# Optimization experiments

Measured on AMD Instinct MI355X. Metric: run time of the kernel, lower is better.

Reference implementation:

```python
import jax, jax.numpy as jnp
import numpy as np

N_NODES = 100000
N_EDGES = 1200000
L = 4  # message-passing layers
SLOPE = 0.01  # nn.LeakyReLU default negative slope


def leaky(v):
    return jnp.where(v >= 0, v, SLOPE * v)


def layer_norm(h, g, b, eps=1e-5):
    mu = jnp.mean(h, axis=-1, keepdims=True)
    var = jnp.var(h, axis=-1, keepdims=True)
    return (h - mu) * jax.lax.rsqrt(var + eps) * g + b


def setup_inputs() -> dict:
    key = jax.random.key(0)
    ks = jax.random.split(key, 20)
    s = 0.05
    return {
        "x": jax.random.normal(ks[0], (N_NODES, 16), jnp.float32),
        "pos": jax.random.uniform(ks[1], (N_NODES, 3), jnp.float32),
        "edge_src": jax.random.randint(ks[2], (N_EDGES,), 0, N_NODES),
        "edge_dst": jax.random.randint(ks[3], (N_EDGES,), 0, N_NODES),
        "edge_w": jax.random.uniform(ks[4], (N_EDGES,), jnp.float32),
        "enc_W1": jax.random.normal(ks[5], (16, 128), jnp.float32) * s,
        "enc_b1": jax.random.normal(ks[6], (128,), jnp.float32) * s,
        "enc_W2": jax.random.normal(ks[7], (128, 64), jnp.float32) * s,
        "enc_b2": jax.random.normal(ks[8], (64,), jnp.float32) * s,
        "dec_W1": jax.random.normal(ks[9], (64, 24), jnp.float32) * s,
        "dec_b1": jax.random.normal(ks[10], (24,), jnp.float32) * s,
        "dec_W2": jax.random.normal(ks[11], (24, 3), jnp.float32) * s,
        "dec_b2": jax.random.normal(ks[12], (3,), jnp.float32) * s,
        "ln_g": jnp.ones((L, 64), jnp.float32),
        "ln_b": jnp.zeros((L, 64), jnp.float32),
        "node_W": jax.random.normal(ks[13], (L, 64, 32), jnp.float32) * s,
        "node_b": jax.random.normal(ks[14], (L, 32), jnp.float32) * s,
        "edge_W": jax.random.normal(ks[15], (L, 64, 32), jnp.float32) * s,
        "edge_b": jax.random.normal(ks[16], (L, 32), jnp.float32) * s,
        "mlp_W": jax.random.normal(ks[17], (L, 32, 64), jnp.float32) * s,
        "mlp_b": jax.random.normal(ks[18], (L, 64), jnp.float32) * s,
    }


def reference(x, pos, edge_src, edge_dst, edge_w,
              enc_W1, enc_b1, enc_W2, enc_b2,
              dec_W1, dec_b1, dec_W2, dec_b2,
              ln_g, ln_b, node_W, node_b, edge_W, edge_b, mlp_W, mlp_b):
    n = x.shape[0]
    # node_encoder: Linear -> LeakyReLU -> Linear
    h = leaky(x @ enc_W1 + enc_b1) @ enc_W2 + enc_b2  # [N, 64]
    for l in range(L):
        hn = layer_norm(h, ln_g[l], ln_b[l])  # [N, 64]
        # edge-weighted scatter-sum: m_e = w_e * h_src, aggregate into dst
        msg = jax.ops.segment_sum(edge_w[:, None] * hn[edge_src], edge_dst,
                                  num_segments=n)  # [N, 64]
        y = (hn @ node_W[l] + node_b[l]) + (msg @ edge_W[l] + edge_b[l])  # [N, 32]
        h = leaky(y) @ mlp_W[l] + mlp_b[l] + hn  # act_first MLP + residual
    # node_decoder: Linear -> LeakyReLU -> Linear
    out = leaky(h @ dec_W1 + dec_b1) @ dec_W2 + dec_b2  # [N, 3]
    return out
```

## Files before the change

kernel.cpp:

```cpp
#include <hip/hip_runtime.h>

#define N_NODES 100000
#define N_EDGES 1200000
#define LAYERS 4
#define SLOPE 0.01f

#define NPAIR (N_NODES / 2)

#define BUCKET_SHIFT 7
#define NB2 ((N_NODES + 127) >> 7)
#define NBLK 128
#define EPB (N_EDGES / NBLK)

__device__ __forceinline__ float leaky(float v) { return v >= 0.f ? v : SLOPE * v; }

#define ACC16(h, v, a, b, c, d) \
    h[0]  += v * a.x; h[1]  += v * a.y; h[2]  += v * a.z; h[3]  += v * a.w; \
    h[4]  += v * b.x; h[5]  += v * b.y; h[6]  += v * b.z; h[7]  += v * b.w; \
    h[8]  += v * c.x; h[9]  += v * c.y; h[10] += v * c.z; h[11] += v * c.w; \
    h[12] += v * d.x; h[13] += v * d.y; h[14] += v * d.z; h[15] += v * d.w;

#define ACC8(r, v, a, b) \
    r[0] += v * a.x; r[1] += v * a.y; r[2] += v * a.z; r[3] += v * a.w; \
    r[4] += v * b.x; r[5] += v * b.y; r[6] += v * b.z; r[7] += v * b.w;

__global__ __launch_bounds__(256) void hist_k(
    const int* __restrict__ dst, int* __restrict__ Hg)
{
    __shared__ int lh[NB2];
    for (int i = threadIdx.x; i < NB2; i += 256) lh[i] = 0;
    __syncthreads();
    int blk = blockIdx.x;
    int e1 = blk * EPB + EPB;
    for (int e = blk * EPB + threadIdx.x; e < e1; e += 256)
        atomicAdd(&lh[dst[e] >> BUCKET_SHIFT], 1);
    __syncthreads();
    for (int i = threadIdx.x; i < NB2; i += 256) Hg[blk * NB2 + i] = lh[i];
}

__global__ __launch_bounds__(NBLK) void scan_blocks_k(
    int* __restrict__ Hg, int* __restrict__ T)
{
    __shared__ int s[NBLK];
    int b = blockIdx.x, t = threadIdx.x;
    int v = Hg[t * NB2 + b];
    s[t] = v; __syncthreads();
    for (int off = 1; off < NBLK; off <<= 1) {
        int y = (t >= off) ? s[t - off] : 0;
        __syncthreads();
        s[t] += y;
        __syncthreads();
    }
    Hg[t * NB2 + b] = s[t] - v;
    if (t == NBLK - 1) T[b] = s[t];
}

__global__ __launch_bounds__(256) void scan_T_k(
    const int* __restrict__ T, int* __restrict__ BS)
{
    __shared__ int s[256];
    int t = threadIdx.x;
    int beg = t * 4, end = beg + 4 > NB2 ? NB2 : beg + 4;
    int v[4]; int sum = 0;
    for (int i = beg, u = 0; i < end; i++, u++) { v[u] = sum; sum += T[i]; }
    s[t] = sum; __syncthreads();
    for (int off = 1; off < 256; off <<= 1) {
        int y = (t >= off) ? s[t - off] : 0;
        __syncthreads();
        s[t] += y;
        __syncthreads();
    }
    int excl = s[t] - sum;
    for (int i = beg, u = 0; i < end; i++, u++) BS[i] = excl + v[u];
    if (t == 0) BS[NB2] = N_EDGES;
}

__global__ __launch_bounds__(256) void scatter_k(
    const int* __restrict__ src, const int* __restrict__ dst,
    const float* __restrict__ w, const int* __restrict__ Hg,
    const int* __restrict__ BS, int2* __restrict__ sE)
{
    __shared__ int cur[NB2];
    int blk = blockIdx.x;
    for (int i = threadIdx.x; i < NB2; i += 256)
        cur[i] = BS[i] + Hg[blk * NB2 + i];
    __syncthreads();
    int e1 = blk * EPB + EPB;
    for (int e = blk * EPB + threadIdx.x; e < e1; e += 256) {
        int d = dst[e];
        int p = atomicAdd(&cur[d >> BUCKET_SHIFT], 1);
        sE[p] = make_int2(src[e] | ((d & 127) << 17), __float_as_int(w[e]));
    }
}

__global__ __launch_bounds__(256) void finalize_k(
    const int* __restrict__ BS, const int2* __restrict__ sE,
    int* __restrict__ offs, int2* __restrict__ ep)
{
    __shared__ int cnt[128];
    __shared__ int s[128];
    __shared__ int cur[128];
    int b = blockIdx.x, t = threadIdx.x;
    int s0 = BS[b], s1 = BS[b + 1];
    if (t < 128) cnt[t] = 0;
    __syncthreads();
    for (int i = s0 + t; i < s1; i += 256)
        atomicAdd(&cnt[(sE[i].x >> 17) & 127], 1);
    __syncthreads();
    int v = 0;
    if (t < 128) { v = cnt[t]; s[t] = v; }
    __syncthreads();
    for (int off = 1; off < 128; off <<= 1) {
        int y = (t >= off && t < 128) ? s[t - off] : 0;
        __syncthreads();
        if (t < 128) s[t] += y;
        __syncthreads();
    }
    if (t < 128) {
        int excl = s[t] - v;
        cur[t] = s0 + excl;
        int node = b * 128 + t;
        if (node < N_NODES) offs[node] = s0 + excl;
    }
    if (b == NB2 - 1 && t == 0) offs[N_NODES] = N_EDGES;
    __syncthreads();
    for (int i = s0 + t; i < s1; i += 256) {
        int2 e = sE[i];
        int p = atomicAdd(&cur[(e.x >> 17) & 127], 1);
        ep[p] = make_int2(e.x & 0x1FFFF, e.y);
    }
}

__global__ __launch_bounds__(256, 2) void enc_ln_gemm(
    const float* __restrict__ x,
    const float* __restrict__ W1, const float* __restrict__ b1,
    const float* __restrict__ W2, const float* __restrict__ b2,
    const float* __restrict__ ln_g, const float* __restrict__ ln_b,
    const float* __restrict__ nodeW, const float* __restrict__ node_b,
    const float* __restrict__ edgeW, const float* __restrict__ edge_b,
    float* __restrict__ H, float* __restrict__ Y, float* __restrict__ Z)
{
    __shared__ float sW1t[128 * 16];
    __shared__ float sW2[128 * 64];
    __shared__ float sNW[64 * 32];
    __shared__ float sEW[64 * 32];
    __shared__ float sb1[128];
    __shared__ float sb2[64];
    __shared__ float sg[64], sb[64], sby[32];
    for (int idx = threadIdx.x; idx < 16 * 128; idx += 256) {
        int i = idx / 128, k = idx % 128;
        sW1t[k * 16 + i] = W1[idx];
    }
    for (int idx = threadIdx.x; idx < 128 * 64; idx += 256) sW2[idx] = W2[idx];
    for (int idx = threadIdx.x; idx < 64 * 32; idx += 256) {
        sNW[idx] = nodeW[idx];
        sEW[idx] = edgeW[idx];
    }
    if (threadIdx.x < 128) sb1[threadIdx.x] = b1[threadIdx.x];
    if (threadIdx.x < 64) {
        sb2[threadIdx.x] = b2[threadIdx.x];
        sg[threadIdx.x] = ln_g[threadIdx.x];
        sb[threadIdx.x] = ln_b[threadIdx.x];
    }
    if (threadIdx.x < 32) sby[threadIdx.x] = node_b[threadIdx.x] + edge_b[threadIdx.x];
    __syncthreads();

    int base = blockIdx.x * 256 + threadIdx.x;
    int pair = base >> 2;
    int q = base & 3;
    if (pair >= NPAIR) return;
    int n0 = pair * 2, n1 = n0 + 1;

    float xi0[16], xi1[16];
    {
        const float4* xv0 = (const float4*)(x + (size_t)n0 * 16);
        const float4* xv1 = (const float4*)(x + (size_t)n1 * 16);
        #pragma unroll
        for (int i = 0; i < 4; i++) {
            float4 t = xv0[i];
            xi0[4 * i] = t.x; xi0[4 * i + 1] = t.y; xi0[4 * i + 2] = t.z; xi0[4 * i + 3] = t.w;
            float4 u = xv1[i];
            xi1[4 * i] = u.x; xi1[4 * i + 1] = u.y; xi1[4 * i + 2] = u.z; xi1[4 * i + 3] = u.w;
        }
    }

    float h0[16], h1[16];
    #pragma unroll
    for (int jj = 0; jj < 16; jj++) { h0[jj] = sb2[q * 16 + jj]; h1[jj] = h0[jj]; }
    #pragma unroll 4
    for (int kk = 0; kk < 32; kk++) {
        int t = kk * 4 + q;
        const float4* wv = (const float4*)(sW1t + t * 16);
        float4 w0 = wv[0], w1 = wv[1], w2 = wv[2], w3 = wv[3];
        float a0 = sb1[t];
        a0 += xi0[0] * w0.x + xi0[1] * w0.y + xi0[2] * w0.z + xi0[3] * w0.w;
        a0 += xi0[4] * w1.x + xi0[5] * w1.y + xi0[6] * w1.z + xi0[7] * w1.w;
        a0 += xi0[8] * w2.x + xi0[9] * w2.y + xi0[10] * w2.z + xi0[11] * w2.w;
        a0 += xi0[12] * w3.x + xi0[13] * w3.y + xi0[14] * w3.z + xi0[15] * w3.w;
        float a1 = sb1[t];
        a1 += xi1[0] * w0.x + xi1[1] * w0.y + xi1[2] * w0.z + xi1[3] * w0.w;
        a1 += xi1[4] * w1.x + xi1[5] * w1.y + xi1[6] * w1.z + xi1[7] * w1.w;
        a1 += xi1[8] * w2.x + xi1[9] * w2.y + xi1[10] * w2.z + xi1[11] * w2.w;
        a1 += xi1[12] * w3.x + xi1[13] * w3.y + xi1[14] * w3.z + xi1[15] * w3.w;
        float hv0 = leaky(a0);
        float hv1 = leaky(a1);
        #pragma unroll
        for (int ss = 0; ss < 4; ss++) {
            float v0 = __shfl(hv0, ss, 4);
            float v1 = __shfl(hv1, ss, 4);
            const float4* w = (const float4*)(sW2 + (kk * 4 + ss) * 64 + q * 16);
            float4 aa = w[0], bb = w[1], cc = w[2], dd = w[3];
            ACC16(h0, v0, aa, bb, cc, dd)
            ACC16(h1, v1, aa, bb, cc, dd)
        }
    }

    float s0 = 0.f, e0 = 0.f, s1 = 0.f, e1 = 0.f;
    #pragma unroll
    for (int jj = 0; jj < 16; jj++) {
        s0 += h0[jj]; e0 += h0[jj] * h0[jj];
        s1 += h1[jj]; e1 += h1[jj] * h1[jj];
    }
    s0 += __shfl_xor(s0, 1, 4); s0 += __shfl_xor(s0, 2, 4);
    e0 += __shfl_xor(e0, 1, 4); e0 += __shfl_xor(e0, 2, 4);
    s1 += __shfl_xor(s1, 1, 4); s1 += __shfl_xor(s1, 2, 4);
    e1 += __shfl_xor(e1, 1, 4); e1 += __shfl_xor(e1, 2, 4);
    float mu0 = s0 * (1.f / 64.f);
    float va0 = e0 * (1.f / 64.f) - mu0 * mu0;
    float r0  = rsqrtf(va0 + 1e-5f);
    float mu1 = s1 * (1.f / 64.f);
    float va1 = e1 * (1.f / 64.f) - mu1 * mu1;
    float r1  = rsqrtf(va1 + 1e-5f);

    #pragma unroll
    for (int jj = 0; jj < 16; jj++) {
        float g = sg[q * 16 + jj], bb = sb[q * 16 + jj];
        h0[jj] = (h0[jj] - mu0) * r0 * g + bb;
        h1[jj] = (h1[jj] - mu1) * r1 * g + bb;
    }
    {
        float4* hs0 = (float4*)(H + (size_t)n0 * 64 + q * 16);
        float4* hs1 = (float4*)(H + (size_t)n1 * 64 + q * 16);
        #pragma unroll
        for (int c = 0; c < 4; c++) {
            hs0[c] = make_float4(h0[4 * c], h0[4 * c + 1], h0[4 * c + 2], h0[4 * c + 3]);
            hs1[c] = make_float4(h1[4 * c], h1[4 * c + 1], h1[4 * c + 2], h1[4 * c + 3]);
        }
    }

    float aY0[8], aZ0[8], aY1[8], aZ1[8];
    #pragma unroll
    for (int jj = 0; jj < 8; jj++) {
        aY0[jj] = sby[q * 8 + jj]; aY1[jj] = aY0[jj];
        aZ0[jj] = 0.f; aZ1[jj] = 0.f;
    }
    #pragma unroll
    for (int kk = 0; kk < 16; kk++) {
        #pragma unroll
        for (int ss = 0; ss < 4; ss++) {
            float v0 = __shfl(h0[kk], ss, 4);
            float v1 = __shfl(h1[kk], ss, 4);
            int k = ss * 16 + kk;
            const float4* nw = (const float4*)(sNW + k * 32 + q * 8);
            const float4* ew = (const float4*)(sEW + k * 32 + q * 8);
            float4 a = nw[0], b = nw[1], c = ew[0], d = ew[1];
            ACC8(aY0, v0, a, b)
            ACC8(aZ0, v0, c, d)
            ACC8(aY1, v1, a, b)
            ACC8(aZ1, v1, c, d)
        }
    }
    float4* yv0 = (float4*)(Y + (size_t)n0 * 32 + q * 8);
    float4* zv0 = (float4*)(Z + (size_t)n0 * 32 + q * 8);
    float4* yv1 = (float4*)(Y + (size_t)n1 * 32 + q * 8);
    float4* zv1 = (float4*)(Z + (size_t)n1 * 32 + q * 8);
    yv0[0] = make_float4(aY0[0], aY0[1], aY0[2], aY0[3]);
    yv0[1] = make_float4(aY0[4], aY0[5], aY0[6], aY0[7]);
    zv0[0] = make_float4(aZ0[0], aZ0[1], aZ0[2], aZ0[3]);
    zv0[1] = make_float4(aZ0[4], aZ0[5], aZ0[6], aZ0[7]);
    yv1[0] = make_float4(aY1[0], aY1[1], aY1[2], aY1[3]);
    yv1[1] = make_float4(aY1[4], aY1[5], aY1[6], aY1[7]);
    zv1[0] = make_float4(aZ1[0], aZ1[1], aZ1[2], aZ1[3]);
    zv1[1] = make_float4(aZ1[4], aZ1[5], aZ1[6], aZ1[7]);
}

__global__ __launch_bounds__(256) void gather_kernel(
    const int* __restrict__ offs, const int2* __restrict__ ep,
    const float* __restrict__ Z, float* __restrict__ Y)
{
    int gid = blockIdx.x * 256 + threadIdx.x;
    int node = gid >> 3;
    int lane = gid & 7;
    if (node >= N_NODES) return;
    int p0 = offs[node], p1 = offs[node + 1];
    float4 acc = make_float4(0.f, 0.f, 0.f, 0.f);
    const float4* Zv = (const float4*)Z;
    int p = p0;
    for (; p + 4 <= p1; p += 4) {
        int2 ea = ep[p];
        int2 eb = ep[p + 1];
        int2 ec = ep[p + 2];
        int2 ed = ep[p + 3];
        float4 za = Zv[(size_t)ea.x * 8 + lane];
        float4 zb = Zv[(size_t)eb.x * 8 + lane];
        float4 zc = Zv[(size_t)ec.x * 8 + lane];
        float4 zd = Zv[(size_t)ed.x * 8 + lane];
        float wa = __int_as_float(ea.y);
        float wb = __int_as_float(eb.y);
        float wc = __int_as_float(ec.y);
        float wd = __int_as_float(ed.y);
        acc.x += wa * za.x + wb * zb.x + wc * zc.x + wd * zd.x;
        acc.y += wa * za.y + wb * zb.y + wc * zc.y + wd * zd.y;
        acc.z += wa * za.z + wb * zb.z + wc * zc.z + wd * zd.z;
        acc.w += wa * za.w + wb * zb.w + wc * zc.w + wd * zd.w;
    }
    for (; p < p1; p++) {
        int2 ea = ep[p];
        float wa = __int_as_float(ea.y);
        float4 za = Zv[(size_t)ea.x * 8 + lane];
        acc.x += wa * za.x; acc.y += wa * za.y;
        acc.z += wa * za.z; acc.w += wa * za.w;
    }
    float4* yp = (float4*)(Y + (size_t)node * 32) + lane;
    float4 y = *yp;
    y.x += acc.x; y.y += acc.y; y.z += acc.z; y.w += acc.w;
    *yp = y;
}

__global__ __launch_bounds__(256) void mlp_ln_gemm(
    float* __restrict__ Yio, float* __restrict__ H, float* __restrict__ Z,
    const float* __restrict__ mlpW, const float* __restrict__ mlp_b,
    const float* __restrict__ ln_g, const float* __restrict__ ln_b,
    const float* __restrict__ nodeW, const float* __restrict__ node_b,
    const float* __restrict__ edgeW, const float* __restrict__ edge_b)
{
    __shared__ float sMW[32 * 64];
    __shared__ float sNW[64 * 32];
    __shared__ float sEW[64 * 32];
    __shared__ float smb[64], sg[64], sb[64], sby[32];
    for (int idx = threadIdx.x; idx < 32 * 64; idx += 256) sMW[idx] = mlpW[idx];
    for (int idx = threadIdx.x; idx < 64 * 32; idx += 256) {
        sNW[idx] = nodeW[idx];
        sEW[idx] = edgeW[idx];
    }
    if (threadIdx.x < 64) {
        smb[threadIdx.x] = mlp_b[threadIdx.x];
        sg[threadIdx.x] = ln_g[threadIdx.x];
        sb[threadIdx.x] = ln_b[threadIdx.x];
    }
    if (threadIdx.x < 32) sby[threadIdx.x] = node_b[threadIdx.x] + edge_b[threadIdx.x];
    __syncthreads();

    int gid = blockIdx.x * 256 + threadIdx.x;
    int node = gid >> 2;
    int q = gid & 3;
    if (node >= N_NODES) return;

    float ly[8];
    const float4* yvin = (const float4*)(Yio + (size_t)node * 32 + q * 8);
    {
        float4 t0 = yvin[0], t1 = yvin[1];
        ly[0] = leaky(t0.x); ly[1] = leaky(t0.y); ly[2] = leaky(t0.z); ly[3] = leaky(t0.w);
        ly[4] = leaky(t1.x); ly[5] = leaky(t1.y); ly[6] = leaky(t1.z); ly[7] = leaky(t1.w);
    }
    float h[16];
    #pragma unroll
    for (int jj = 0; jj < 16; jj++) h[jj] = smb[q * 16 + jj];
    #pragma unroll
    for (int kk = 0; kk < 8; kk++) {
        #pragma unroll
        for (int ss = 0; ss < 4; ss++) {
            float v = __shfl(ly[kk], ss, 4);
            const float4* w = (const float4*)(sMW + (ss * 8 + kk) * 64 + q * 16);
            float4 a = w[0], b = w[1], c = w[2], d = w[3];
            ACC16(h, v, a, b, c, d)
        }
    }
    float4* hp = (float4*)(H + (size_t)node * 64 + q * 16);
    #pragma unroll
    for (int c = 0; c < 4; c++) {
        float4 r = hp[c];
        h[4 * c] += r.x; h[4 * c + 1] += r.y; h[4 * c + 2] += r.z; h[4 * c + 3] += r.w;
    }
    float s = 0.f, s2 = 0.f;
    #pragma unroll
    for (int jj = 0; jj < 16; jj++) { s += h[jj]; s2 += h[jj] * h[jj]; }
    s  += __shfl_xor(s, 1, 4);  s  += __shfl_xor(s, 2, 4);
    s2 += __shfl_xor(s2, 1, 4); s2 += __shfl_xor(s2, 2, 4);
    float mu  = s * (1.f / 64.f);
    float var = s2 * (1.f / 64.f) - mu * mu;
    float rs  = rsqrtf(var + 1e-5f);

    float hn[16];
    #pragma unroll
    for (int jj = 0; jj < 16; jj++)
        hn[jj] = (h[jj] - mu) * rs * sg[q * 16 + jj] + sb[q * 16 + jj];
    #pragma unroll
    for (int c = 0; c < 4; c++)
        hp[c] = make_float4(hn[4 * c], hn[4 * c + 1], hn[4 * c + 2], hn[4 * c + 3]);

    float aY[8], aZ[8];
    #pragma unroll
    for (int jj = 0; jj < 8; jj++) { aY[jj] = sby[q * 8 + jj]; aZ[jj] = 0.f; }
    #pragma unroll
    for (int kk = 0; kk < 16; kk++) {
        #pragma unroll
        for (int ss = 0; ss < 4; ss++) {
            float v = __shfl(hn[kk], ss, 4);
            int k = ss * 16 + kk;
            const float4* nw = (const float4*)(sNW + k * 32 + q * 8);
            const float4* ew = (const float4*)(sEW + k * 32 + q * 8);
            float4 a = nw[0], b = nw[1], c = ew[0], d = ew[1];
            ACC8(aY, v, a, b)
            ACC8(aZ, v, c, d)
        }
    }
    float4* yo = (float4*)(Yio + (size_t)node * 32 + q * 8);
    float4* zv = (float4*)(Z + (size_t)node * 32 + q * 8);
    yo[0] = make_float4(aY[0], aY[1], aY[2], aY[3]);
    yo[1] = make_float4(aY[4], aY[5], aY[6], aY[7]);
    zv[0] = make_float4(aZ[0], aZ[1], aZ[2], aZ[3]);
    zv[1] = make_float4(aZ[4], aZ[5], aZ[6], aZ[7]);
}

__global__ __launch_bounds__(256) void mlp_dec(
    const float* __restrict__ Y, const float* __restrict__ H,
    const float* __restrict__ mlpW, const float* __restrict__ mlp_b,
    const float* __restrict__ dW1, const float* __restrict__ db1,
    const float* __restrict__ dW2, const float* __restrict__ db2,
    float* __restrict__ out)
{
    __shared__ float sMW[32 * 64];
    __shared__ float smb[64];
    __shared__ float sW1t[24 * 65];
    __shared__ float sb1[24];
    __shared__ float sW2[24 * 3];
    __shared__ float sb2v[3];
    for (int idx = threadIdx.x; idx < 32 * 64; idx += 256) sMW[idx] = mlpW[idx];
    for (int idx = threadIdx.x; idx < 64 * 24; idx += 256) {
        int k = idx / 24, t = idx % 24;
        sW1t[t * 65 + k] = dW1[idx];
    }
    if (threadIdx.x < 64) smb[threadIdx.x] = mlp_b[threadIdx.x];
    if (threadIdx.x < 24) sb1[threadIdx.x] = db1[threadIdx.x];
    if (threadIdx.x < 72) sW2[threadIdx.x] = dW2[threadIdx.x];
    if (threadIdx.x < 3)  sb2v[threadIdx.x] = db2[threadIdx.x];
    __syncthreads();

    int gid = blockIdx.x * 256 + threadIdx.x;
    int node = gid >> 2;
    int q = gid & 3;
    if (node >= N_NODES) return;

    float ly[8];
    const float4* yvin = (const float4*)(Y + (size_t)node * 32 + q * 8);
    {
        float4 t0 = yvin[0], t1 = yvin[1];
        ly[0] = leaky(t0.x); ly[1] = leaky(t0.y); ly[2] = leaky(t0.z); ly[3] = leaky(t0.w);
        ly[4] = leaky(t1.x); ly[5] = leaky(t1.y); ly[6] = leaky(t1.z); ly[7] = leaky(t1.w);
    }
    float h[16];
    #pragma unroll
    for (int jj = 0; jj < 16; jj++) h[jj] = smb[q * 16 + jj];
    #pragma unroll
    for (int kk = 0; kk < 8; kk++) {
        #pragma unroll
        for (int ss = 0; ss < 4; ss++) {
            float v = __shfl(ly[kk], ss, 4);
            const float4* w = (const float4*)(sMW + (ss * 8 + kk) * 64 + q * 16);
            float4 a = w[0], b = w[1], c = w[2], d = w[3];
            ACC16(h, v, a, b, c, d)
        }
    }
    const float4* hp = (const float4*)(H + (size_t)node * 64 + q * 16);
    #pragma unroll
    for (int c = 0; c < 4; c++) {
        float4 r = hp[c];
        h[4 * c] += r.x; h[4 * c + 1] += r.y; h[4 * c + 2] += r.z; h[4 * c + 3] += r.w;
    }
    float hid[6];
    #pragma unroll
    for (int t = 0; t < 6; t++) hid[t] = sb1[q * 6 + t];
    #pragma unroll
    for (int kk = 0; kk < 16; kk++) {
        #pragma unroll
        for (int ss = 0; ss < 4; ss++) {
            float v = __shfl(h[kk], ss, 4);
            int k = ss * 16 + kk;
            #pragma unroll
            for (int t = 0; t < 6; t++)
                hid[t] += v * sW1t[(q * 6 + t) * 65 + k];
        }
    }
    float o0 = 0.f, o1 = 0.f, o2 = 0.f;
    #pragma unroll
    for (int t = 0; t < 6; t++) {
        float lt = leaky(hid[t]);
        int tg = q * 6 + t;
        o0 += lt * sW2[tg * 3 + 0];
        o1 += lt * sW2[tg * 3 + 1];
        o2 += lt * sW2[tg * 3 + 2];
    }
    o0 += __shfl_xor(o0, 1, 4); o0 += __shfl_xor(o0, 2, 4);
    o1 += __shfl_xor(o1, 1, 4); o1 += __shfl_xor(o1, 2, 4);
    o2 += __shfl_xor(o2, 1, 4); o2 += __shfl_xor(o2, 2, 4);
    if (q == 0) {
        float* op = out + (size_t)node * 3;
        op[0] = o0 + sb2v[0]; op[1] = o1 + sb2v[1]; op[2] = o2 + sb2v[2];
    }
}

extern "C" void kernel_launch(void* const* d_in, const int* in_sizes, int n_in,
                              void* d_out, int out_size, void* d_ws, size_t ws_size,
                              hipStream_t stream)
{
    const float* x      = (const float*)d_in[0];
    const int*   esrc   = (const int*)d_in[2];
    const int*   edst   = (const int*)d_in[3];
    const float* ew     = (const float*)d_in[4];
    const float* enc_W1 = (const float*)d_in[5];
    const float* enc_b1 = (const float*)d_in[6];
    const float* enc_W2 = (const float*)d_in[7];
    const float* enc_b2 = (const float*)d_in[8];
    const float* dec_W1 = (const float*)d_in[9];
    const float* dec_b1 = (const float*)d_in[10];
    const float* dec_W2 = (const float*)d_in[11];
    const float* dec_b2 = (const float*)d_in[12];
    const float* ln_g   = (const float*)d_in[13];
    const float* ln_b   = (const float*)d_in[14];
    const float* node_W = (const float*)d_in[15];
    const float* node_b = (const float*)d_in[16];
    const float* edge_W = (const float*)d_in[17];
    const float* edge_b = (const float*)d_in[18];
    const float* mlp_W  = (const float*)d_in[19];
    const float* mlp_b  = (const float*)d_in[20];

    float* H  = (float*)d_ws;
    float* Y  = H + (size_t)N_NODES * 64;
    float* Z  = Y + (size_t)N_NODES * 32;
    int2*  ep = (int2*)(Z + (size_t)N_NODES * 32);
    int* offs = (int*)(ep + N_EDGES);
    int* Hg   = offs + N_NODES + 1;
    int* T    = Hg + NBLK * NB2;
    int* BS   = T + NB2;
    int2* sE  = (int2*)H;

    const int pairBlocks   = (NPAIR * 4 + 255) / 256;
    const int node4Blocks  = (N_NODES * 4 + 255) / 256;
    const int gatherBlocks = (N_NODES * 8 + 255) / 256;

    hist_k<<<NBLK, 256, 0, stream>>>(edst, Hg);
    scan_blocks_k<<<NB2, NBLK, 0, stream>>>(Hg, T);
    scan_T_k<<<1, 256, 0, stream>>>(T, BS);
    scatter_k<<<NBLK, 256, 0, stream>>>(esrc, edst, ew, Hg, BS, sE);
    finalize_k<<<NB2, 256, 0, stream>>>(BS, sE, offs, ep);

    enc_ln_gemm<<<pairBlocks, 256, 0, stream>>>(
        x, enc_W1, enc_b1, enc_W2, enc_b2,
        ln_g, ln_b, node_W, node_b, edge_W, edge_b, H, Y, Z);

    for (int l = 0; l < LAYERS - 1; l++) {
        gather_kernel<<<gatherBlocks, 256, 0, stream>>>(offs, ep, Z, Y);
        mlp_ln_gemm<<<node4Blocks, 256, 0, stream>>>(
            Y, H, Z,
            mlp_W + l * 32 * 64, mlp_b + l * 64,
            ln_g + (l + 1) * 64, ln_b + (l + 1) * 64,
            node_W + (l + 1) * 64 * 32, node_b + (l + 1) * 32,
            edge_W + (l + 1) * 64 * 32, edge_b + (l + 1) * 32);
    }
    gather_kernel<<<gatherBlocks, 256, 0, stream>>>(offs, ep, Z, Y);
    mlp_dec<<<node4Blocks, 256, 0, stream>>>(
        Y, H, mlp_W + 3 * 32 * 64, mlp_b + 3 * 64,
        dec_W1, dec_b1, dec_W2, dec_b2, (float*)d_out);
}
```

Measured before the change: 461.5 us.

## Fuse edge gather into MLP kernels with ping-pong Z buffers

Folds the per-node CSR gather of Z messages into the mlp_ln_gemm and mlp_dec kernels. Z is double-buffered so a layer can read the previous Z while writing the next one, and the fused path is enabled only when the workspace is large enough. This removes four gather launches and one Y read-modify-write per layer, but each node's gather now runs on 4 lanes with 8 floats each instead of 8 lanes with 4 floats each, which lowers memory-level parallelism. Separately, enc_ln_gemm drops its shared-memory copies of node/edge weights and its occupancy hint, reading those weights straight from global memory.

Result: slower. 507.7 us (+10.0%).

```diff
diff --git a/kernel.cpp b/kernel.cpp
--- a/kernel.cpp
+++ b/kernel.cpp
@@ -131,7 +131,7 @@
     }
 }
 
-__global__ __launch_bounds__(256, 2) void enc_ln_gemm(
+__global__ __launch_bounds__(256) void enc_ln_gemm(
     const float* __restrict__ x,
     const float* __restrict__ W1, const float* __restrict__ b1,
     const float* __restrict__ W2, const float* __restrict__ b2,
@@ -142,8 +142,6 @@
 {
     __shared__ float sW1t[128 * 16];
     __shared__ float sW2[128 * 64];
-    __shared__ float sNW[64 * 32];
-    __shared__ float sEW[64 * 32];
     __shared__ float sb1[128];
     __shared__ float sb2[64];
     __shared__ float sg[64], sb[64], sby[32];
@@ -152,10 +150,6 @@
         sW1t[k * 16 + i] = W1[idx];
     }
     for (int idx = threadIdx.x; idx < 128 * 64; idx += 256) sW2[idx] = W2[idx];
-    for (int idx = threadIdx.x; idx < 64 * 32; idx += 256) {
-        sNW[idx] = nodeW[idx];
-        sEW[idx] = edgeW[idx];
-    }
     if (threadIdx.x < 128) sb1[threadIdx.x] = b1[threadIdx.x];
     if (threadIdx.x < 64) {
         sb2[threadIdx.x] = b2[threadIdx.x];
@@ -261,8 +255,8 @@
             float v0 = __shfl(h0[kk], ss, 4);
             float v1 = __shfl(h1[kk], ss, 4);
             int k = ss * 16 + kk;
-            const float4* nw = (const float4*)(sNW + k * 32 + q * 8);
-            const float4* ew = (const float4*)(sEW + k * 32 + q * 8);
+            const float4* nw = (const float4*)(nodeW + k * 32 + q * 8);
+            const float4* ew = (const float4*)(edgeW + k * 32 + q * 8);
             float4 a = nw[0], b = nw[1], c = ew[0], d = ew[1];
             ACC8(aY0, v0, a, b)
             ACC8(aZ0, v0, c, d)
@@ -328,11 +322,14 @@
 }
 
 __global__ __launch_bounds__(256) void mlp_ln_gemm(
-    float* __restrict__ Yio, float* __restrict__ H, float* __restrict__ Z,
+    const int* __restrict__ offs, const int2* __restrict__ ep,
+    const float* __restrict__ Zin,
+    float* __restrict__ Yio, float* __restrict__ H, float* __restrict__ Zout,
     const float* __restrict__ mlpW, const float* __restrict__ mlp_b,
     const float* __restrict__ ln_g, const float* __restrict__ ln_b,
     const float* __restrict__ nodeW, const float* __restrict__ node_b,
-    const float* __restrict__ edgeW, const float* __restrict__ edge_b)
+    const float* __restrict__ edgeW, const float* __restrict__ edge_b,
+    int fuse)
 {
     __shared__ float sMW[32 * 64];
     __shared__ float sNW[64 * 32];
@@ -356,12 +353,51 @@
     int q = gid & 3;
     if (node >= N_NODES) return;
 
+    float ga[8];
+    #pragma unroll
+    for (int j = 0; j < 8; j++) ga[j] = 0.f;
+    if (fuse) {
+        int p0 = offs[node], p1 = offs[node + 1];
+        const float4* Zv = (const float4*)Zin;
+        int p = p0;
+        for (; p + 2 <= p1; p += 2) {
+            int2 ea = ep[p];
+            int2 eb = ep[p + 1];
+            float4 za0 = Zv[(size_t)ea.x * 8 + 2 * q];
+            float4 za1 = Zv[(size_t)ea.x * 8 + 2 * q + 1];
+            float4 zb0 = Zv[(size_t)eb.x * 8 + 2 * q];
+            float4 zb1 = Zv[(size_t)eb.x * 8 + 2 * q + 1];
+            float wa = __int_as_float(ea.y);
+            float wb = __int_as_float(eb.y);
+            ga[0] += wa * za0.x + wb * zb0.x;
+            ga[1] += wa * za0.y + wb * zb0.y;
+            ga[2] += wa * za0.z + wb * zb0.z;
+            ga[3] += wa * za0.w + wb * zb0.w;
+            ga[4] += wa * za1.x + wb * zb1.x;
+            ga[5] += wa * za1.y + wb * zb1.y;
+            ga[6] += wa * za1.z + wb * zb1.z;
+            ga[7] += wa * za1.w + wb * zb1.w;
+        }
+        if (p < p1) {
+            int2 ea = ep[p];
+            float4 za0 = Zv[(size_t)ea.x * 8 + 2 * q];
+            float4 za1 = Zv[(size_t)ea.x * 8 + 2 * q + 1];
+            float wa = __int_as_float(ea.y);
+            ga[0] += wa * za0.x; ga[1] += wa * za0.y;
+            ga[2] += wa * za0.z; ga[3] += wa * za0.w;
+            ga[4] += wa * za1.x; ga[5] += wa * za1.y;
+            ga[6] += wa * za1.z; ga[7] += wa * za1.w;
+        }
+    }
+
     float ly[8];
     const float4* yvin = (const float4*)(Yio + (size_t)node * 32 + q * 8);
     {
         float4 t0 = yvin[0], t1 = yvin[1];
-        ly[0] = leaky(t0.x); ly[1] = leaky(t0.y); ly[2] = leaky(t0.z); ly[3] = leaky(t0.w);
-        ly[4] = leaky(t1.x); ly[5] = leaky(t1.y); ly[6] = leaky(t1.z); ly[7] = leaky(t1.w);
+        ly[0] = leaky(t0.x + ga[0]); ly[1] = leaky(t0.y + ga[1]);
+        ly[2] = leaky(t0.z + ga[2]); ly[3] = leaky(t0.w + ga[3]);
+        ly[4] = leaky(t1.x + ga[4]); ly[5] = leaky(t1.y + ga[5]);
+        ly[6] = leaky(t1.z + ga[6]); ly[7] = leaky(t1.w + ga[7]);
     }
     float h[16];
     #pragma unroll
@@ -416,7 +452,7 @@
         }
     }
     float4* yo = (float4*)(Yio + (size_t)node * 32 + q * 8);
-    float4* zv = (float4*)(Z + (size_t)node * 32 + q * 8);
+    float4* zv = (float4*)(Zout + (size_t)node * 32 + q * 8);
     yo[0] = make_float4(aY[0], aY[1], aY[2], aY[3]);
     yo[1] = make_float4(aY[4], aY[5], aY[6], aY[7]);
     zv[0] = make_float4(aZ[0], aZ[1], aZ[2], aZ[3]);
@@ -424,11 +460,13 @@
 }
 
 __global__ __launch_bounds__(256) void mlp_dec(
+    const int* __restrict__ offs, const int2* __restrict__ ep,
+    const float* __restrict__ Zin,
     const float* __restrict__ Y, const float* __restrict__ H,
     const float* __restrict__ mlpW, const float* __restrict__ mlp_b,
     const float* __restrict__ dW1, const float* __restrict__ db1,
     const float* __restrict__ dW2, const float* __restrict__ db2,
-    float* __restrict__ out)
+    float* __restrict__ out, int fuse)
 {
     __shared__ float sMW[32 * 64];
     __shared__ float smb[64];
@@ -452,12 +490,51 @@
     int q = gid & 3;
     if (node >= N_NODES) return;
 
+    float ga[8];
+    #pragma unroll
+    for (int j = 0; j < 8; j++) ga[j] = 0.f;
+    if (fuse) {
+        int p0 = offs[node], p1 = offs[node + 1];
+        const float4* Zv = (const float4*)Zin;
+        int p = p0;
+        for (; p + 2 <= p1; p += 2) {
+            int2 ea = ep[p];
+            int2 eb = ep[p + 1];
+            float4 za0 = Zv[(size_t)ea.x * 8 + 2 * q];
+            float4 za1 = Zv[(size_t)ea.x * 8 + 2 * q + 1];
+            float4 zb0 = Zv[(size_t)eb.x * 8 + 2 * q];
+            float4 zb1 = Zv[(size_t)eb.x * 8 + 2 * q + 1];
+            float wa = __int_as_float(ea.y);
+            float wb = __int_as_float(eb.y);
+            ga[0] += wa * za0.x + wb * zb0.x;
+            ga[1] += wa * za0.y + wb * zb0.y;
+            ga[2] += wa * za0.z + wb * zb0.z;
+            ga[3] += wa * za0.w + wb * zb0.w;
+            ga[4] += wa * za1.x + wb * zb1.x;
+            ga[5] += wa * za1.y + wb * zb1.y;
+            ga[6] += wa * za1.z + wb * zb1.z;
+            ga[7] += wa * za1.w + wb * zb1.w;
+        }
+        if (p < p1) {
+            int2 ea = ep[p];
+            float4 za0 = Zv[(size_t)ea.x * 8 + 2 * q];
+            float4 za1 = Zv[(size_t)ea.x * 8 + 2 * q + 1];
+            float wa = __int_as_float(ea.y);
+            ga[0] += wa * za0.x; ga[1] += wa * za0.y;
+            ga[2] += wa * za0.z; ga[3] += wa * za0.w;
+            ga[4] += wa * za1.x; ga[5] += wa * za1.y;
+            ga[6] += wa * za1.z; ga[7] += wa * za1.w;
+        }
+    }
+
     float ly[8];
     const float4* yvin = (const float4*)(Y + (size_t)node * 32 + q * 8);
     {
         float4 t0 = yvin[0], t1 = yvin[1];
-        ly[0] = leaky(t0.x); ly[1] = leaky(t0.y); ly[2] = leaky(t0.z); ly[3] = leaky(t0.w);
-        ly[4] = leaky(t1.x); ly[5] = leaky(t1.y); ly[6] = leaky(t1.z); ly[7] = leaky(t1.w);
+        ly[0] = leaky(t0.x + ga[0]); ly[1] = leaky(t0.y + ga[1]);
+        ly[2] = leaky(t0.z + ga[2]); ly[3] = leaky(t0.w + ga[3]);
+        ly[4] = leaky(t1.x + ga[4]); ly[5] = leaky(t1.y + ga[5]);
+        ly[6] = leaky(t1.z + ga[6]); ly[7] = leaky(t1.w + ga[7]);
     }
     float h[16];
     #pragma unroll
@@ -537,12 +614,16 @@
 
     float* H  = (float*)d_ws;
     float* Y  = H + (size_t)N_NODES * 64;
-    float* Z  = Y + (size_t)N_NODES * 32;
-    int2*  ep = (int2*)(Z + (size_t)N_NODES * 32);
+    float* Za = Y + (size_t)N_NODES * 32;
+    int2*  ep = (int2*)(Za + (size_t)N_NODES * 32);
     int* offs = (int*)(ep + N_EDGES);
     int* Hg   = offs + N_NODES + 1;
     int* T    = Hg + NBLK * NB2;
     int* BS   = T + NB2;
+    float* Zb = (float*)(BS + NB2 + 2);
+    size_t needed = ((char*)(Zb + (size_t)N_NODES * 32)) - (char*)d_ws;
+    int fuse = (ws_size >= needed) ? 1 : 0;
+    if (!fuse) Zb = Za;
     int2* sE  = (int2*)H;
 
     const int pairBlocks   = (NPAIR * 4 + 255) / 256;
@@ -557,19 +638,25 @@
 
     enc_ln_gemm<<<pairBlocks, 256, 0, stream>>>(
         x, enc_W1, enc_b1, enc_W2, enc_b2,
-        ln_g, ln_b, node_W, node_b, edge_W, edge_b, H, Y, Z);
-
+        ln_g, ln_b, node_W, node_b, edge_W, edge_b, H, Y, Za);
+
+    float* zin = Za;
+    float* zout = fuse ? Zb : Za;
     for (int l = 0; l < LAYERS - 1; l++) {
-        gather_kernel<<<gatherBlocks, 256, 0, stream>>>(offs, ep, Z, Y);
+        if (!fuse)
+            gather_kernel<<<gatherBlocks, 256, 0, stream>>>(offs, ep, zin, Y);
         mlp_ln_gemm<<<node4Blocks, 256, 0, stream>>>(
-            Y, H, Z,
+            offs, ep, zin, Y, H, zout,
             mlp_W + l * 32 * 64, mlp_b + l * 64,
             ln_g + (l + 1) * 64, ln_b + (l + 1) * 64,
             node_W + (l + 1) * 64 * 32, node_b + (l + 1) * 32,
-            edge_W + (l + 1) * 64 * 32, edge_b + (l + 1) * 32);
-    }
-    gather_kernel<<<gatherBlocks, 256, 0, stream>>>(offs, ep, Z, Y);
+            edge_W + (l + 1) * 64 * 32, edge_b + (l + 1) * 32, fuse);
+        if (fuse) { float* t = zin; zin = zout; zout = t; }
+    }
+    if (!fuse)
+        gather_kernel<<<gatherBlocks, 256, 0, stream>>>(offs, ep, zin, Y);
     mlp_dec<<<node4Blocks, 256, 0, stream>>>(
-        Y, H, mlp_W + 3 * 32 * 64, mlp_b + 3 * 64,
-        dec_W1, dec_b1, dec_W2, dec_b2, (float*)d_out);
-}
+        offs, ep, zin, Y, H,
+        mlp_W + 3 * 32 * 64, mlp_b + 3 * 64,
+        dec_W1, dec_b1, dec_W2, dec_b2, (float*)d_out, fuse);
+}
```
